# Kernel optimization log

Hardware: AMD Instinct MI355X
Metric: run time of the kernel (lower is better)

Reference implementation:

```python
import jax, jax.numpy as jnp
import numpy as np

EPS = 1e-5


def conv2d(x, w, b, stride=1, pad=1):
    out = jax.lax.conv_general_dilated(
        x, w, (stride, stride), [(pad, pad), (pad, pad)],
        dimension_numbers=('NCHW', 'OIHW', 'NCHW'))
    return out + b[None, :, None, None]


def bn_inf(x, gamma, beta, mean, var):
    inv = gamma / jnp.sqrt(var + EPS)
    return x * inv[None, :, None, None] + (beta - mean * inv)[None, :, None, None]


def deform_conv(x, offset, weight, stride, pad, dil):
    # x: [B,Ci,H,W], offset: [B,2*K*K,Ho,Wo] (dy,dx interleaved per kernel pos),
    # weight: [Co,Ci,K,K]. torchvision DeformConv2d v1 semantics, no bias.
    B, Ci, H, W = x.shape
    Co, _, K, _ = weight.shape
    KK = K * K
    Ho = (H + 2 * pad - dil * (K - 1) - 1) // stride + 1
    Wo = (W + 2 * pad - dil * (K - 1) - 1) // stride + 1
    dy = offset[:, 0::2]  # [B,KK,Ho,Wo]
    dx = offset[:, 1::2]
    ky, kx = jnp.meshgrid(jnp.arange(K), jnp.arange(K), indexing='ij')
    ky = ky.reshape(KK).astype(x.dtype)
    kx = kx.reshape(KK).astype(x.dtype)
    base_y = (jnp.arange(Ho) * stride - pad).astype(x.dtype)
    base_x = (jnp.arange(Wo) * stride - pad).astype(x.dtype)
    ys = base_y[None, None, :, None] + (ky * dil)[None, :, None, None] + dy
    xs = base_x[None, None, None, :] + (kx * dil)[None, :, None, None] + dx
    y0 = jnp.floor(ys)
    x0 = jnp.floor(xs)
    fy = ys - y0
    fx = xs - x0

    def gather(img, iy, ix):
        # img: [Ci,H,W]; iy, ix: [KK,Ho,Wo] float integer-valued coords
        valid = (iy >= 0) & (iy < H) & (ix >= 0) & (ix < W)
        iyc = jnp.clip(iy, 0, H - 1).astype(jnp.int32)
        ixc = jnp.clip(ix, 0, W - 1).astype(jnp.int32)
        v = img[:, iyc, ixc]  # [Ci,KK,Ho,Wo]
        return v * valid[None].astype(img.dtype)

    def sample_one(img, y0b, x0b, fyb, fxb):
        w00 = (1 - fyb) * (1 - fxb)
        w01 = (1 - fyb) * fxb
        w10 = fyb * (1 - fxb)
        w11 = fyb * fxb
        s = (gather(img, y0b, x0b) * w00[None]
             + gather(img, y0b, x0b + 1) * w01[None]
             + gather(img, y0b + 1, x0b) * w10[None]
             + gather(img, y0b + 1, x0b + 1) * w11[None])
        return s  # [Ci,KK,Ho,Wo]

    sampled = jax.vmap(sample_one)(x, y0, x0, fy, fx)  # [B,Ci,KK,Ho,Wo]
    return jnp.einsum('oik,bikhw->bohw', weight.reshape(Co, Ci, KK), sampled)


def setup_inputs() -> dict:
    key = jax.random.key(0)
    ks = jax.random.split(key, 16)
    B, C, H, W = 8, 128, 64, 64
    d = dict(
        x=jax.random.normal(ks[0], (B, C, H, W), jnp.float32),
        w_off1=jax.random.normal(ks[1], (18, C, 3, 3), jnp.float32) * 0.01,
        b_off1=jnp.zeros((18,), jnp.float32),
        w_dc1=jax.random.normal(ks[2], (C, C, 3, 3), jnp.float32) * 0.05,
        g1=jnp.ones((C,), jnp.float32),
        beta1=jnp.zeros((C,), jnp.float32),
        m1=jax.random.normal(ks[3], (C,), jnp.float32) * 0.1,
        v1=jax.random.uniform(ks[4], (C,), jnp.float32) + 0.5,
        w_off2=jax.random.normal(ks[5], (18, C, 3, 3), jnp.float32) * 0.01,
        b_off2=jnp.zeros((18,), jnp.float32),
        w_dc2=jax.random.normal(ks[6], (C, C, 3, 3), jnp.float32) * 0.05,
        g2=jnp.ones((C,), jnp.float32),
        beta2=jnp.zeros((C,), jnp.float32),
        m2=jax.random.normal(ks[7], (C,), jnp.float32) * 0.1,
        v2=jax.random.uniform(ks[8], (C,), jnp.float32) + 0.5,
    )
    return d


def reference(x, w_off1, b_off1, w_dc1, g1, beta1, m1, v1,
              w_off2, b_off2, w_dc2, g2, beta2, m2, v2):
    # BasicBlock6 forward (stride=1, in_planes==planes => identity shortcut)
    off1 = conv2d(x, w_off1, b_off1, stride=1, pad=1)
    out = jax.nn.relu(bn_inf(deform_conv(x, off1, w_dc1, 1, 2, 2), g1, beta1, m1, v1))
    off2 = conv2d(out, w_off2, b_off2, stride=1, pad=1)
    out = bn_inf(deform_conv(out, off2, w_dc2, 1, 2, 2), g2, beta2, m2, v2)
    out = out + x  # identity shortcut
    return jax.nn.relu(out)
```

## Files before the change

kernel.cpp:

```cpp
#include <hip/hip_runtime.h>
#include <hip/hip_bf16.h>

#define CH   128
#define HH   64
#define WW   64
#define OFFC 18

typedef __attribute__((ext_vector_type(8))) short bf16x8;
typedef __attribute__((ext_vector_type(4))) short bf16x4;
typedef __attribute__((ext_vector_type(4))) float f32x4;

static __device__ __forceinline__ unsigned short f2bf(float f) {
    __hip_bfloat16 h = __float2bfloat16(f);
    return *reinterpret_cast<unsigned short*>(&h);
}
static __device__ __forceinline__ float bf2f(unsigned short u) {
    union { unsigned int i; float f; } x; x.i = ((unsigned int)u) << 16;
    return x.f;
}

__global__ __launch_bounds__(256) void pack_all_kernel(
    const float* __restrict__ wdc1, const float* __restrict__ wdc2,
    const float* __restrict__ wof1, const float* __restrict__ wof2,
    unsigned short* __restrict__ wpk1, unsigned short* __restrict__ wpk2,
    unsigned short* __restrict__ wpo1, unsigned short* __restrict__ wpo2)
{
    int blk = blockIdx.x;
    int tid = threadIdx.x;
    if (blk < 1152) {
        const float* w = (blk < 576) ? wdc1 : wdc2;
        unsigned short* wp = (blk < 576) ? wpk1 : wpk2;
        int id = (blk % 576) * 256 + tid;
        int j    = id & 7;
        int lane = (id >> 3) & 63;
        int ot   = (id >> 9) & 7;
        int kk   = (id >> 12) & 3;
        int k    = id >> 14;
        int o = ot * 16 + (lane & 15);
        int i = kk * 32 + (lane >> 4) * 8 + j;
        wp[id] = f2bf(w[(o * CH + i) * 9 + k]);
    } else {
        const float* w = (blk < 1296) ? wof1 : wof2;
        unsigned short* wp = (blk < 1296) ? wpo1 : wpo2;
        int id = ((blk - 1152) % 144) * 256 + tid;
        int j    = id & 7;
        int lane = (id >> 3) & 63;
        int mt   = (id >> 9) & 1;
        int kk   = (id >> 10) & 3;
        int k    = id >> 12;
        int o = mt * 16 + (lane & 15);
        int i = kk * 32 + (lane >> 4) * 8 + j;
        wp[id] = (o < OFFC) ? f2bf(w[(o * CH + i) * 9 + k]) : (unsigned short)0;
    }
}

__global__ __launch_bounds__(256) void to_nhwc_kernel(
    const float* __restrict__ x, unsigned short* __restrict__ xh)
{
    __shared__ float s[CH][WW + 1];
    int blk = blockIdx.x;
    int tid = threadIdx.x;
    const float* xb = x + ((size_t)(blk >> 6) * CH * HH + (blk & 63)) * WW;

    int c_off = tid >> 4, w0 = (tid & 15) * 4;
    #pragma unroll
    for (int it = 0; it < 8; ++it) {
        int c = it * 16 + c_off;
        float4 vv = *(const float4*)&xb[(size_t)c * HH * WW + w0];
        s[c][w0] = vv.x; s[c][w0 + 1] = vv.y; s[c][w0 + 2] = vv.z; s[c][w0 + 3] = vv.w;
    }
    __syncthreads();

    int w = tid & 63, c0 = (tid >> 6) * 32;
    unsigned short* dst = xh + ((size_t)blk * WW + w) * CH + c0;
    unsigned short tmp[32];
    #pragma unroll
    for (int j = 0; j < 32; ++j) tmp[j] = f2bf(s[c0 + j][w]);
    #pragma unroll
    for (int q = 0; q < 4; ++q)
        *(bf16x8*)(dst + q * 8) = *(const bf16x8*)(tmp + q * 8);
}

__global__ __launch_bounds__(256) void off_conv_mfma_kernel(
    const unsigned short* __restrict__ xh,
    const unsigned short* __restrict__ wpo,
    const float* __restrict__ bias,
    unsigned short* __restrict__ offh)
{
    int wgid = blockIdx.x;
    int blk  = (wgid & 7) * 64 + (wgid >> 3);
    int b = blk >> 6, oh = blk & 63;
    int tid = threadIdx.x;
    int lane = tid & 63;
    int nt = tid >> 6;
    int nl = lane & 15;
    int kg = lane >> 4;

    f32x4 acc0 = {0.f, 0.f, 0.f, 0.f}, acc1 = {0.f, 0.f, 0.f, 0.f};
    const unsigned short* xb = xh + (size_t)b * HH * WW * CH;

    for (int k = 0; k < 9; ++k) {
        int ky = k / 3, kx = k - ky * 3;
        int ih = oh - 1 + ky;
        if (ih < 0 || ih >= HH) continue;
        int iw = nt * 16 + nl + kx - 1;
        bool valid = (iw >= 0) && (iw < WW);
        const unsigned short* row = xb + ((size_t)ih * WW + (valid ? iw : 0)) * CH + kg * 8;
        const unsigned short* wk = wpo + (size_t)k * 8 * 512;
        #pragma unroll
        for (int kk = 0; kk < 4; ++kk) {
            bf16x8 bfrag = {0, 0, 0, 0, 0, 0, 0, 0};
            if (valid) bfrag = *(const bf16x8*)(row + kk * 32);
            bf16x8 a0 = *(const bf16x8*)(wk + (kk * 2 + 0) * 512 + lane * 8);
            bf16x8 a1 = *(const bf16x8*)(wk + (kk * 2 + 1) * 512 + lane * 8);
            acc0 = __builtin_amdgcn_mfma_f32_16x16x32_bf16(a0, bfrag, acc0, 0, 0, 0);
            acc1 = __builtin_amdgcn_mfma_f32_16x16x32_bf16(a1, bfrag, acc1, 0, 0, 0);
        }
    }

    int ow = nt * 16 + nl;
    #pragma unroll
    for (int r = 0; r < 4; ++r) {
        int co = kg * 4 + r;
        offh[(((size_t)b * OFFC + co) * HH + oh) * WW + ow] = f2bf(acc0[r] + bias[co]);
    }
    if (kg == 0) {
        #pragma unroll
        for (int r = 0; r < 2; ++r) {
            int co = 16 + r;
            offh[(((size_t)b * OFFC + co) * HH + oh) * WW + ow] = f2bf(acc1[r] + bias[co]);
        }
    }
}

__global__ __launch_bounds__(256) void deform_mfma2_kernel(
    const unsigned short* __restrict__ xh,
    const unsigned short* __restrict__ offh,
    const unsigned short* __restrict__ wpk,
    const float* __restrict__ g, const float* __restrict__ beta,
    const float* __restrict__ m, const float* __restrict__ v,
    const float* __restrict__ residual,
    unsigned short* __restrict__ out_h,
    float* __restrict__ out_f)
{
    __shared__ unsigned short sB[32 * 128];

    int wgid = blockIdx.x;
    int blk  = (wgid & 7) * 128 + (wgid >> 3);
    int owh = blk & 1, oh = (blk >> 1) & 63, b = blk >> 7;
    int ow0 = owh * 32;
    int tid = threadIdx.x, lane = tid & 63, wv = tid >> 6;

    int s_ow = tid >> 3;
    int ci0  = (tid & 7) * 16;
    int ow_g = ow0 + s_ow;

    const unsigned short* xb = xh + (size_t)b * HH * WW * CH;

    f32x4 acc[2][2];
    #pragma unroll
    for (int a = 0; a < 2; ++a)
        #pragma unroll
        for (int q = 0; q < 2; ++q) acc[a][q] = (f32x4){0.f, 0.f, 0.f, 0.f};

    for (int k = 0; k < 9; ++k) {
        int ky = k / 3, kx = k - ky * 3;

        float dy = bf2f(offh[(((size_t)b * OFFC + 2 * k) * HH + oh) * WW + ow_g]);
        float dx = bf2f(offh[(((size_t)b * OFFC + 2 * k + 1) * HH + oh) * WW + ow_g]);
        float ys = (float)(oh - 2 + ky * 2) + dy;
        float xs = (float)(ow_g - 2 + kx * 2) + dx;
        float y0f = floorf(ys), x0f = floorf(xs);
        float fy = ys - y0f, fx = xs - x0f;
        int y0 = (int)y0f, x0 = (int)x0f;
        int y1 = y0 + 1,   x1 = x0 + 1;
        bool vy0 = (y0 >= 0) & (y0 < HH);
        bool vy1 = (y1 >= 0) & (y1 < HH);
        bool vx0 = (x0 >= 0) & (x0 < WW);
        bool vx1 = (x1 >= 0) & (x1 < WW);
        int y0c = min(max(y0, 0), HH - 1), y1c = min(max(y1, 0), HH - 1);
        int x0c = min(max(x0, 0), WW - 1), x1c = min(max(x1, 0), WW - 1);
        float cw0 = (1.f - fy) * (1.f - fx) * ((vy0 && vx0) ? 1.f : 0.f);
        float cw1 = (1.f - fy) * fx         * ((vy0 && vx1) ? 1.f : 0.f);
        float cw2 = fy * (1.f - fx)         * ((vy1 && vx0) ? 1.f : 0.f);
        float cw3 = fy * fx                 * ((vy1 && vx1) ? 1.f : 0.f);

        const unsigned short* p0 = xb + ((size_t)(y0c * WW + x0c)) * CH + ci0;
        const unsigned short* p1 = xb + ((size_t)(y0c * WW + x1c)) * CH + ci0;
        const unsigned short* p2 = xb + ((size_t)(y1c * WW + x0c)) * CH + ci0;
        const unsigned short* p3 = xb + ((size_t)(y1c * WW + x1c)) * CH + ci0;

        bf16x8 v00 = *(const bf16x8*)(p0),     v01 = *(const bf16x8*)(p0 + 8);
        bf16x8 v10 = *(const bf16x8*)(p1),     v11 = *(const bf16x8*)(p1 + 8);
        bf16x8 v20 = *(const bf16x8*)(p2),     v21 = *(const bf16x8*)(p2 + 8);
        bf16x8 v30 = *(const bf16x8*)(p3),     v31 = *(const bf16x8*)(p3 + 8);

        union { bf16x8 v8; unsigned short u[8]; } w0, w1;
        #pragma unroll
        for (int j = 0; j < 8; ++j) {
            float a0 = cw0 * bf2f((unsigned short)v00[j])
                     + cw1 * bf2f((unsigned short)v10[j])
                     + cw2 * bf2f((unsigned short)v20[j])
                     + cw3 * bf2f((unsigned short)v30[j]);
            float a1 = cw0 * bf2f((unsigned short)v01[j])
                     + cw1 * bf2f((unsigned short)v11[j])
                     + cw2 * bf2f((unsigned short)v21[j])
                     + cw3 * bf2f((unsigned short)v31[j]);
            w0.u[j] = f2bf(a0);
            w1.u[j] = f2bf(a1);
        }
        int base = s_ow * 256 + ci0 * 2;
        int swz  = (s_ow & 7) << 4;
        *(bf16x8*)((char*)sB + ( base       ^ swz)) = w0.v8;
        *(bf16x8*)((char*)sB + ((base + 16) ^ swz)) = w1.v8;
        __syncthreads();

        const unsigned short* wk = wpk + (size_t)k * 16384;
        #pragma unroll
        for (int kk = 0; kk < 4; ++kk) {
            bf16x8 a0 = *(const bf16x8*)(wk + (kk * 8 + 2 * wv)     * 512 + lane * 8);
            bf16x8 a1 = *(const bf16x8*)(wk + (kk * 8 + 2 * wv + 1) * 512 + lane * 8);
            #pragma unroll
            for (int owt = 0; owt < 2; ++owt) {
                int owl = owt * 16 + (lane & 15);
                int rbyte = (owl * 256 + (kk * 32 + (lane >> 4) * 8) * 2)
                            ^ ((owl & 7) << 4);
                bf16x8 bf = *(const bf16x8*)((const char*)sB + rbyte);
                acc[0][owt] = __builtin_amdgcn_mfma_f32_16x16x32_bf16(
                                  a0, bf, acc[0][owt], 0, 0, 0);
                acc[1][owt] = __builtin_amdgcn_mfma_f32_16x16x32_bf16(
                                  a1, bf, acc[1][owt], 0, 0, 0);
            }
        }
        __syncthreads();
    }

    if (out_h != nullptr) {
        #pragma unroll
        for (int otl = 0; otl < 2; ++otl) {
            int ob = (2 * wv + otl) * 16 + (lane >> 4) * 4;
            float inv[4], sh[4];
            #pragma unroll
            for (int r = 0; r < 4; ++r) {
                int o = ob + r;
                float iv = g[o] / sqrtf(v[o] + 1e-5f);
                inv[r] = iv; sh[r] = beta[o] - m[o] * iv;
            }
            #pragma unroll
            for (int owt = 0; owt < 2; ++owt) {
                int ow = ow0 + owt * 16 + (lane & 15);
                union { bf16x4 v4; unsigned short u[4]; } pk;
                #pragma unroll
                for (int r = 0; r < 4; ++r) {
                    float val = acc[otl][owt][r] * inv[r] + sh[r];
                    pk.u[r] = f2bf(fmaxf(val, 0.f));
                }
                *(bf16x4*)(out_h + ((size_t)(b * HH + oh) * WW + ow) * CH + ob) = pk.v4;
            }
        }
    } else {
        #pragma unroll
        for (int otl = 0; otl < 2; ++otl) {
            #pragma unroll
            for (int r = 0; r < 4; ++r) {
                int o = (2 * wv + otl) * 16 + (lane >> 4) * 4 + r;
                float iv = g[o] / sqrtf(v[o] + 1e-5f);
                float sh = beta[o] - m[o] * iv;
                #pragma unroll
                for (int owt = 0; owt < 2; ++owt) {
                    int ow = ow0 + owt * 16 + (lane & 15);
                    size_t idx = (((size_t)b * CH + o) * HH + oh) * WW + ow;
                    float val = acc[otl][owt][r] * iv + sh + residual[idx];
                    out_f[idx] = fmaxf(val, 0.f);
                }
            }
        }
    }
}

extern "C" void kernel_launch(void* const* d_in, const int* in_sizes, int n_in,
                              void* d_out, int out_size, void* d_ws, size_t ws_size,
                              hipStream_t stream)
{
    const float* x      = (const float*)d_in[0];
    const float* w_off1 = (const float*)d_in[1];
    const float* b_off1 = (const float*)d_in[2];
    const float* w_dc1  = (const float*)d_in[3];
    const float* g1     = (const float*)d_in[4];
    const float* beta1  = (const float*)d_in[5];
    const float* m1     = (const float*)d_in[6];
    const float* v1     = (const float*)d_in[7];
    const float* w_off2 = (const float*)d_in[8];
    const float* b_off2 = (const float*)d_in[9];
    const float* w_dc2  = (const float*)d_in[10];
    const float* g2     = (const float*)d_in[11];
    const float* beta2  = (const float*)d_in[12];
    const float* m2     = (const float*)d_in[13];
    const float* v2     = (const float*)d_in[14];
    float* out = (float*)d_out;

    char* ws = (char*)d_ws;
    unsigned short* xh    = (unsigned short*)ws;
    unsigned short* out1h = (unsigned short*)(ws + 8388608);
    unsigned short* offh  = (unsigned short*)(ws + 16777216);
    unsigned short* wpk1  = (unsigned short*)(ws + 17956864);
    unsigned short* wpk2  = (unsigned short*)(ws + 18251776);
    unsigned short* wpo1  = (unsigned short*)(ws + 18546688);
    unsigned short* wpo2  = (unsigned short*)(ws + 18620416);

    pack_all_kernel<<<1440, 256, 0, stream>>>(w_dc1, w_dc2, w_off1, w_off2,
                                              wpk1, wpk2, wpo1, wpo2);
    to_nhwc_kernel<<<512, 256, 0, stream>>>(x, xh);

    off_conv_mfma_kernel<<<512, 256, 0, stream>>>(xh, wpo1, b_off1, offh);
    deform_mfma2_kernel<<<1024, 256, 0, stream>>>(xh, offh, wpk1,
                                                  g1, beta1, m1, v1,
                                                  nullptr, out1h, nullptr);
    off_conv_mfma_kernel<<<512, 256, 0, stream>>>(out1h, wpo2, b_off2, offh);
    deform_mfma2_kernel<<<1024, 256, 0, stream>>>(out1h, offh, wpk2,
                                                  g2, beta2, m2, v2,
                                                  x, nullptr, out);
}
```

Baseline: 101.5 us.

## Merge prep kernels, stage deform offsets in LDS, and split gather into halves

Merges the weight-packing and NHWC conversion kernels into one launch, which removes one kernel launch. In the deform kernel, all 18 offset channels for the tile are preloaded into shared memory before the k loop, replacing scattered global loads inside the loop. The bilinear gather now loads and blends one 8-channel half at a time to reduce live registers, and launch bounds request 4 blocks per SM. The trade-offs are a larger shared-memory footprint in the prep kernel's weight-packing blocks and an extra barrier at the start of the deform kernel.

Result: faster. 96.69 us (-4.7%).

```diff
diff --git a/kernel.cpp b/kernel.cpp
--- a/kernel.cpp
+++ b/kernel.cpp
@@ -19,14 +19,17 @@
     return x.f;
 }
 
-__global__ __launch_bounds__(256) void pack_all_kernel(
+__global__ __launch_bounds__(256) void prep_kernel(
+    const float* __restrict__ x, unsigned short* __restrict__ xh,
     const float* __restrict__ wdc1, const float* __restrict__ wdc2,
     const float* __restrict__ wof1, const float* __restrict__ wof2,
     unsigned short* __restrict__ wpk1, unsigned short* __restrict__ wpk2,
     unsigned short* __restrict__ wpo1, unsigned short* __restrict__ wpo2)
 {
+    __shared__ float s[CH][WW + 1];
     int blk = blockIdx.x;
     int tid = threadIdx.x;
+
     if (blk < 1152) {
         const float* w = (blk < 576) ? wdc1 : wdc2;
         unsigned short* wp = (blk < 576) ? wpk1 : wpk2;
@@ -39,7 +42,9 @@
         int o = ot * 16 + (lane & 15);
         int i = kk * 32 + (lane >> 4) * 8 + j;
         wp[id] = f2bf(w[(o * CH + i) * 9 + k]);
-    } else {
+        return;
+    }
+    if (blk < 1440) {
         const float* w = (blk < 1296) ? wof1 : wof2;
         unsigned short* wp = (blk < 1296) ? wpo1 : wpo2;
         int id = ((blk - 1152) % 144) * 256 + tid;
@@ -51,16 +56,11 @@
         int o = mt * 16 + (lane & 15);
         int i = kk * 32 + (lane >> 4) * 8 + j;
         wp[id] = (o < OFFC) ? f2bf(w[(o * CH + i) * 9 + k]) : (unsigned short)0;
-    }
-}
-
-__global__ __launch_bounds__(256) void to_nhwc_kernel(
-    const float* __restrict__ x, unsigned short* __restrict__ xh)
-{
-    __shared__ float s[CH][WW + 1];
-    int blk = blockIdx.x;
-    int tid = threadIdx.x;
-    const float* xb = x + ((size_t)(blk >> 6) * CH * HH + (blk & 63)) * WW;
+        return;
+    }
+
+    int nb = blk - 1440;
+    const float* xb = x + ((size_t)(nb >> 6) * CH * HH + (nb & 63)) * WW;
 
     int c_off = tid >> 4, w0 = (tid & 15) * 4;
     #pragma unroll
@@ -72,7 +72,7 @@
     __syncthreads();
 
     int w = tid & 63, c0 = (tid >> 6) * 32;
-    unsigned short* dst = xh + ((size_t)blk * WW + w) * CH + c0;
+    unsigned short* dst = xh + ((size_t)nb * WW + w) * CH + c0;
     unsigned short tmp[32];
     #pragma unroll
     for (int j = 0; j < 32; ++j) tmp[j] = f2bf(s[c0 + j][w]);
@@ -106,7 +106,7 @@
         int iw = nt * 16 + nl + kx - 1;
         bool valid = (iw >= 0) && (iw < WW);
         const unsigned short* row = xb + ((size_t)ih * WW + (valid ? iw : 0)) * CH + kg * 8;
-        const unsigned short* wk = wpo + (size_t)k * 8 * 512;
+        const unsigned short* wk = wpo + (size_t)k * 4096;
         #pragma unroll
         for (int kk = 0; kk < 4; ++kk) {
             bf16x8 bfrag = {0, 0, 0, 0, 0, 0, 0, 0};
@@ -133,7 +133,7 @@
     }
 }
 
-__global__ __launch_bounds__(256) void deform_mfma2_kernel(
+__global__ __launch_bounds__(256, 4) void deform_mfma2_kernel(
     const unsigned short* __restrict__ xh,
     const unsigned short* __restrict__ offh,
     const unsigned short* __restrict__ wpk,
@@ -144,6 +144,7 @@
     float* __restrict__ out_f)
 {
     __shared__ unsigned short sB[32 * 128];
+    __shared__ float off_s[2 * 9][32];
 
     int wgid = blockIdx.x;
     int blk  = (wgid & 7) * 128 + (wgid >> 3);
@@ -157,6 +158,13 @@
 
     const unsigned short* xb = xh + (size_t)b * HH * WW * CH;
 
+    for (int i = tid; i < 2 * 9 * 32; i += 256) {
+        int co = i >> 5, owl = i & 31;
+        off_s[co][owl] =
+            bf2f(offh[(((size_t)b * OFFC + co) * HH + oh) * WW + ow0 + owl]);
+    }
+    __syncthreads();
+
     f32x4 acc[2][2];
     #pragma unroll
     for (int a = 0; a < 2; ++a)
@@ -166,20 +174,18 @@
     for (int k = 0; k < 9; ++k) {
         int ky = k / 3, kx = k - ky * 3;
 
-        float dy = bf2f(offh[(((size_t)b * OFFC + 2 * k) * HH + oh) * WW + ow_g]);
-        float dx = bf2f(offh[(((size_t)b * OFFC + 2 * k + 1) * HH + oh) * WW + ow_g]);
+        float dy = off_s[2 * k][s_ow];
+        float dx = off_s[2 * k + 1][s_ow];
         float ys = (float)(oh - 2 + ky * 2) + dy;
         float xs = (float)(ow_g - 2 + kx * 2) + dx;
         float y0f = floorf(ys), x0f = floorf(xs);
         float fy = ys - y0f, fx = xs - x0f;
-        int y0 = (int)y0f, x0 = (int)x0f;
-        int y1 = y0 + 1,   x1 = x0 + 1;
-        bool vy0 = (y0 >= 0) & (y0 < HH);
-        bool vy1 = (y1 >= 0) & (y1 < HH);
-        bool vx0 = (x0 >= 0) & (x0 < WW);
-        bool vx1 = (x1 >= 0) & (x1 < WW);
+        int y0 = (int)y0f, x0i = (int)x0f;
+        int y1 = y0 + 1, x1 = x0i + 1;
+        bool vy0 = (y0 >= 0) & (y0 < HH), vy1 = (y1 >= 0) & (y1 < HH);
+        bool vx0 = (x0i >= 0) & (x0i < WW), vx1 = (x1 >= 0) & (x1 < WW);
         int y0c = min(max(y0, 0), HH - 1), y1c = min(max(y1, 0), HH - 1);
-        int x0c = min(max(x0, 0), WW - 1), x1c = min(max(x1, 0), WW - 1);
+        int x0c = min(max(x0i, 0), WW - 1), x1c = min(max(x1, 0), WW - 1);
         float cw0 = (1.f - fy) * (1.f - fx) * ((vy0 && vx0) ? 1.f : 0.f);
         float cw1 = (1.f - fy) * fx         * ((vy0 && vx1) ? 1.f : 0.f);
         float cw2 = fy * (1.f - fx)         * ((vy1 && vx0) ? 1.f : 0.f);
@@ -190,29 +196,25 @@
         const unsigned short* p2 = xb + ((size_t)(y1c * WW + x0c)) * CH + ci0;
         const unsigned short* p3 = xb + ((size_t)(y1c * WW + x1c)) * CH + ci0;
 
-        bf16x8 v00 = *(const bf16x8*)(p0),     v01 = *(const bf16x8*)(p0 + 8);
-        bf16x8 v10 = *(const bf16x8*)(p1),     v11 = *(const bf16x8*)(p1 + 8);
-        bf16x8 v20 = *(const bf16x8*)(p2),     v21 = *(const bf16x8*)(p2 + 8);
-        bf16x8 v30 = *(const bf16x8*)(p3),     v31 = *(const bf16x8*)(p3 + 8);
-
-        union { bf16x8 v8; unsigned short u[8]; } w0, w1;
-        #pragma unroll
-        for (int j = 0; j < 8; ++j) {
-            float a0 = cw0 * bf2f((unsigned short)v00[j])
-                     + cw1 * bf2f((unsigned short)v10[j])
-                     + cw2 * bf2f((unsigned short)v20[j])
-                     + cw3 * bf2f((unsigned short)v30[j]);
-            float a1 = cw0 * bf2f((unsigned short)v01[j])
-                     + cw1 * bf2f((unsigned short)v11[j])
-                     + cw2 * bf2f((unsigned short)v21[j])
-                     + cw3 * bf2f((unsigned short)v31[j]);
-            w0.u[j] = f2bf(a0);
-            w1.u[j] = f2bf(a1);
-        }
         int base = s_ow * 256 + ci0 * 2;
         int swz  = (s_ow & 7) << 4;
-        *(bf16x8*)((char*)sB + ( base       ^ swz)) = w0.v8;
-        *(bf16x8*)((char*)sB + ((base + 16) ^ swz)) = w1.v8;
+        #pragma unroll
+        for (int q = 0; q < 2; ++q) {
+            bf16x8 g0 = *(const bf16x8*)(p0 + q * 8);
+            bf16x8 g1 = *(const bf16x8*)(p1 + q * 8);
+            bf16x8 g2 = *(const bf16x8*)(p2 + q * 8);
+            bf16x8 g3 = *(const bf16x8*)(p3 + q * 8);
+            union { bf16x8 v8; unsigned short u[8]; } wu;
+            #pragma unroll
+            for (int j = 0; j < 8; ++j) {
+                float val = cw0 * bf2f((unsigned short)g0[j])
+                          + cw1 * bf2f((unsigned short)g1[j])
+                          + cw2 * bf2f((unsigned short)g2[j])
+                          + cw3 * bf2f((unsigned short)g3[j]);
+                wu.u[j] = f2bf(val);
+            }
+            *(bf16x8*)((char*)sB + ((base + q * 16) ^ swz)) = wu.v8;
+        }
         __syncthreads();
 
         const unsigned short* wk = wpk + (size_t)k * 16384;
@@ -225,11 +227,11 @@
                 int owl = owt * 16 + (lane & 15);
                 int rbyte = (owl * 256 + (kk * 32 + (lane >> 4) * 8) * 2)
                             ^ ((owl & 7) << 4);
-                bf16x8 bf = *(const bf16x8*)((const char*)sB + rbyte);
+                bf16x8 bfv = *(const bf16x8*)((const char*)sB + rbyte);
                 acc[0][owt] = __builtin_amdgcn_mfma_f32_16x16x32_bf16(
-                                  a0, bf, acc[0][owt], 0, 0, 0);
+                                  a0, bfv, acc[0][owt], 0, 0, 0);
                 acc[1][owt] = __builtin_amdgcn_mfma_f32_16x16x32_bf16(
-                                  a1, bf, acc[1][owt], 0, 0, 0);
+                                  a1, bfv, acc[1][owt], 0, 0, 0);
             }
         }
         __syncthreads();
@@ -308,9 +310,8 @@
     unsigned short* wpo1  = (unsigned short*)(ws + 18546688);
     unsigned short* wpo2  = (unsigned short*)(ws + 18620416);
 
-    pack_all_kernel<<<1440, 256, 0, stream>>>(w_dc1, w_dc2, w_off1, w_off2,
-                                              wpk1, wpk2, wpo1, wpo2);
-    to_nhwc_kernel<<<512, 256, 0, stream>>>(x, xh);
+    prep_kernel<<<1952, 256, 0, stream>>>(x, xh, w_dc1, w_dc2, w_off1, w_off2,
+                                          wpk1, wpk2, wpo1, wpo2);
 
     off_conv_mfma_kernel<<<512, 256, 0, stream>>>(xh, wpo1, b_off1, offh);
     deform_mfma2_kernel<<<1024, 256, 0, stream>>>(xh, offh, wpk1,
```
